# Optimization experiments

Measured on AMD Instinct MI355X. Metric: run time of the kernel, lower is better.

## Reference

```python
import jax, jax.numpy as jnp
import numpy as np

B, C, H, W = 8, 128, 64, 64
INTER = C // 2

def setup_inputs() -> dict:
    key = jax.random.key(0)
    ks = jax.random.split(key, 9)
    s = 0.05
    return {
        "x": jax.random.normal(ks[0], (B, C, H, W), dtype=jnp.float32),
        "theta_w": jax.random.normal(ks[1], (INTER, C), dtype=jnp.float32) * s,
        "theta_b": jax.random.normal(ks[2], (INTER,), dtype=jnp.float32) * s,
        "phi_w": jax.random.normal(ks[3], (INTER, C), dtype=jnp.float32) * s,
        "phi_b": jax.random.normal(ks[4], (INTER,), dtype=jnp.float32) * s,
        "g_w": jax.random.normal(ks[5], (INTER, C), dtype=jnp.float32) * s,
        "g_b": jax.random.normal(ks[6], (INTER,), dtype=jnp.float32) * s,
        "out_w": jax.random.normal(ks[7], (C, INTER), dtype=jnp.float32) * s,
        "out_b": jax.random.normal(ks[8], (C,), dtype=jnp.float32) * s,
    }

def reference(x, theta_w, theta_b, phi_w, phi_b, g_w, g_b, out_w, out_b):
    b, c, h, w = x.shape
    xf = x.reshape(b, c, h * w)                                   # [b, C, n]
    # 1x1 convs == per-pixel channel matmuls
    theta = jnp.einsum('oc,bcn->bno', theta_w, xf) + theta_b       # [b, n, inter]
    phi = jnp.einsum('oc,bcn->bon', phi_w, xf) + phi_b[:, None]    # [b, inter, n]
    g = jnp.einsum('oc,bcn->bno', g_w, xf) + g_b                   # [b, n, inter]
    attn = jax.nn.softmax(jnp.einsum('bno,bom->bnm', theta, phi), axis=-1)  # [b, n, n]
    y = jnp.einsum('bnm,bmo->bon', attn, g)                        # [b, inter, n]
    out = jnp.einsum('oc,bcn->bon', out_w, y) + out_b[:, None]     # [b, C, n]
    return out.reshape(b, c, h, w) + x
```

## Files before the change

kernel.cpp:

```cpp
#include <hip/hip_runtime.h>
#include <hip/hip_bf16.h>
#include <cstdint>
#include <cmath>

#define N_PIX 4096
#define CH    128
#define DD    64
#define NBATCH 8
#define NT    32

typedef unsigned short u16;
typedef __attribute__((ext_vector_type(8))) short bf8_t;
typedef __attribute__((ext_vector_type(4))) float f4_t;
typedef __attribute__((ext_vector_type(16))) float f16v;
typedef uint32_t u32x4 __attribute__((ext_vector_type(4)));
typedef uint32_t u32x2 __attribute__((ext_vector_type(2)));

#define L2E 1.44269504088896340736f

#if __has_builtin(__builtin_amdgcn_exp2f)
  #define EXP2(x) __builtin_amdgcn_exp2f(x)
#else
  #define EXP2(x) exp2f(x)
#endif

__device__ __forceinline__ u16 f2b(float f) {
  return __builtin_bit_cast(u16, __float2bfloat16(f));
}
__device__ __forceinline__ float b2f(u16 h) {
  union { uint32_t u; float f; } v; v.u = ((uint32_t)h) << 16;
  return v.f;
}
__device__ __forceinline__ uint32_t pack2(float a, float b) {
  return (uint32_t)f2b(a) | ((uint32_t)f2b(b) << 16);
}
__device__ __forceinline__ float max3f(float a, float b, float c) {
  return fmaxf(fmaxf(a, b), c);
}
__device__ __forceinline__ f4_t mfma16(bf8_t a, bf8_t b, f4_t c) {
  return __builtin_amdgcn_mfma_f32_16x16x32_bf16(a, b, c, 0, 0, 0);
}
__device__ __forceinline__ f16v mfma32(bf8_t a, bf8_t b, f16v c) {
  return __builtin_amdgcn_mfma_f32_32x32x16_bf16(a, b, c, 0, 0, 0);
}
__device__ __forceinline__ void pl32swap(uint32_t &a, uint32_t &b) {
  u32x2 r = __builtin_amdgcn_permlane32_swap(a, b, false, false);
  a = r[0];
  b = r[1];
}

__global__ __launch_bounds__(256) void proj_kernel(
    const float* __restrict__ x,
    const float* __restrict__ tw, const float* __restrict__ tb,
    const float* __restrict__ pw, const float* __restrict__ pb,
    const float* __restrict__ gw, const float* __restrict__ gb,
    u16* __restrict__ theta_h, u16* __restrict__ phi_h, u16* __restrict__ gt_h) {
  __shared__ __align__(16) u16 xT[64][136];
  const int blk = blockIdx.x;
  const int b  = blk >> 6;
  const int n0 = (blk & 63) << 6;
  const int tid = threadIdx.x;

  #pragma unroll
  for (int i = 0; i < 8; ++i) {
    int idx = tid + i * 256;
    int px = (idx & 15) * 4;
    int c  = idx >> 4;
    float4 v = *(const float4*)(x + ((size_t)b * CH + c) * N_PIX + n0 + px);
    xT[px + 0][c] = f2b(v.x);
    xT[px + 1][c] = f2b(v.y);
    xT[px + 2][c] = f2b(v.z);
    xT[px + 3][c] = f2b(v.w);
  }
  __syncthreads();

  const int lane = tid & 63;
  const int w    = tid >> 6;
  const int l4   = lane >> 4, l15 = lane & 15;

  bf8_t bw[3][4];
  float bias[3];
  #pragma unroll
  for (int nt = 0; nt < 3; ++nt) {
    int op = 16 * (3 * w + nt) + l15;
    const float* wrow; float bv; float scl;
    if (op < 64)       { wrow = tw + op * CH;          bv = tb[op];        scl = L2E; }
    else if (op < 128) { wrow = pw + (op - 64) * CH;   bv = pb[op - 64];   scl = 1.f; }
    else               { wrow = gw + (op - 128) * CH;  bv = gb[op - 128];  scl = 1.f; }
    bias[nt] = bv * scl;
    #pragma unroll
    for (int ks = 0; ks < 4; ++ks) {
      const float* p = wrow + 32 * ks + l4 * 8;
      bf8_t v;
      #pragma unroll
      for (int j = 0; j < 8; ++j) v[j] = (short)f2b(p[j] * scl);
      bw[nt][ks] = v;
    }
  }

  f4_t acc[4][3];
  #pragma unroll
  for (int mt = 0; mt < 4; ++mt)
    #pragma unroll
    for (int nt = 0; nt < 3; ++nt) acc[mt][nt] = (f4_t){0.f, 0.f, 0.f, 0.f};

  #pragma unroll
  for (int mt = 0; mt < 4; ++mt) {
    #pragma unroll
    for (int ks = 0; ks < 4; ++ks) {
      bf8_t a = *(const bf8_t*)&xT[l15 + 16 * mt][32 * ks + l4 * 8];
      #pragma unroll
      for (int nt = 0; nt < 3; ++nt)
        acc[mt][nt] = mfma16(a, bw[nt][ks], acc[mt][nt]);
    }
  }

  #pragma unroll
  for (int nt = 0; nt < 3; ++nt) {
    int op = 16 * (3 * w + nt) + l15;
    #pragma unroll
    for (int mt = 0; mt < 4; ++mt) {
      #pragma unroll
      for (int r = 0; r < 4; ++r) {
        int q = n0 + 16 * mt + l4 * 4 + r;
        u16 h = f2b(acc[mt][nt][r] + bias[nt]);
        if (op < 64)       theta_h[((size_t)b * N_PIX + q) * DD + op] = h;
        else if (op < 128) phi_h[((size_t)b * N_PIX + q) * DD + (op - 64)] = h;
        else               gt_h[((size_t)b * DD + (op - 128)) * N_PIX + q] = h;
      }
    }
  }
}

__global__ __launch_bounds__(512, 4) void attn_kernel(
    const u16* __restrict__ theta_h, const u16* __restrict__ phi_h,
    const u16* __restrict__ gt_h, u16* __restrict__ y_h) {
  __shared__ __align__(16) u16 smem[32768];

  const int bid = blockIdx.x;
  const int lb  = (bid & 7) * 64 + (bid >> 3);
  const int b   = lb >> 6;
  const int q0  = (lb & 63) << 6;
  const int tid = threadIdx.x;
  const int l   = tid & 63;
  const int w   = tid >> 6;
  const int qg  = w & 1;
  const int mh  = w >> 1;
  const int l31 = l & 31;
  const int hi  = l >> 5;

  bf8_t th[4];
  {
    const u16* trow = theta_h + ((size_t)b * N_PIX + q0 + 32 * qg + l31) * DD;
    #pragma unroll
    for (int kk = 0; kk < 4; ++kk)
      th[kk] = *(const bf8_t*)(trow + 16 * kk + 8 * hi);
  }

  const bf8_t onesA = __builtin_bit_cast(bf8_t,
      (u32x4){0x3F803F80u, 0x3F803F80u, 0x3F803F80u, 0x3F803F80u});

  f16v yacc[2];
  #pragma unroll
  for (int ot = 0; ot < 2; ++ot)
    #pragma unroll
    for (int r = 0; r < 16; ++r) yacc[ot][r] = 0.f;
  f16v y2;
  #pragma unroll
  for (int r = 0; r < 16; ++r) y2[r] = 0.f;
  float m_ = -1e30f;

  const int pr  = tid >> 3, pc = tid & 7;
  const int go  = tid >> 4, gc = tid & 15;
  const u16* phA = phi_h + ((size_t)b * N_PIX + pr) * DD + pc * 8;
  const u16* gtA = gt_h + ((size_t)b * DD + go) * N_PIX + gc * 8;
  const int pO0 = pr * 64 + ((pc ^ (pr & 7)) << 3);
  const int pO1 = pO0 + 4096;
  const int gO0 = 8192 + go * 128 + ((gc ^ (go & 7)) << 3);
  const int gO1 = gO0 + 4096;

  uint4 v0, v1, v2, v3;
  #define LOADS(kb_) do {                                              \
    v0 = *(const uint4*)(phA + (size_t)(kb_) * 8192);                  \
    v1 = *(const uint4*)(phA + (size_t)(kb_) * 8192 + 4096);           \
    v2 = *(const uint4*)(gtA + (size_t)(kb_) * 128);                   \
    v3 = *(const uint4*)(gtA + (size_t)(kb_) * 128 + 32 * (size_t)N_PIX); \
  } while (0)
  #define WRITES(buf_) do {                                            \
    u16* base_ = smem + (buf_) * 16384;                                \
    *(uint4*)(base_ + pO0) = v0;                                       \
    *(uint4*)(base_ + pO1) = v1;                                       \
    *(uint4*)(base_ + gO0) = v2;                                       \
    *(uint4*)(base_ + gO1) = v3;                                       \
  } while (0)

  LOADS(0); WRITES(0);
  __syncthreads();

  const int prow  = 32 * mh + l31;
  const int pbase = prow * 64;
  const int pkey  = prow & 7;

  #pragma unroll 2
  for (int t = 0; t < NT; ++t) {
    const int cur = t & 1;
    if (t < NT - 1) LOADS(t + 1);
    const u16* pb = smem + cur * 16384;
    const u16* gb = pb + 8192;

    f16v st;
    #pragma unroll
    for (int r = 0; r < 16; ++r) st[r] = 0.f;
    __builtin_amdgcn_s_setprio(1);
    #pragma unroll
    for (int kk = 0; kk < 4; ++kk) {
      bf8_t a = *(const bf8_t*)(pb + pbase + (((2 * kk + hi) ^ pkey) << 3));
      st = mfma32(a, th[kk], st);
    }
    __builtin_amdgcn_s_setprio(0);

    float t0 = max3f(st[0],  st[1],  st[2]);
    float t1 = max3f(st[3],  st[4],  st[5]);
    float t2 = max3f(st[6],  st[7],  st[8]);
    float t3 = max3f(st[9],  st[10], st[11]);
    float t4 = max3f(st[12], st[13], st[14]);
    float pmax = fmaxf(max3f(t0, t1, t2), max3f(t3, t4, st[15]));
    pmax = fmaxf(pmax, __shfl_xor(pmax, 32));

    if (!__all(pmax <= m_ + 8.f)) {
      float mn = fmaxf(m_, pmax);
      float sc = EXP2(m_ - mn);
      m_ = mn;
      y2[0] *= sc;
      #pragma unroll
      for (int ot = 0; ot < 2; ++ot)
        #pragma unroll
        for (int r = 0; r < 16; ++r) yacc[ot][r] *= sc;
    }

    #pragma unroll
    for (int r = 0; r < 16; ++r) st[r] = EXP2(st[r] - m_);

    uint32_t c0 = pack2(st[0],  st[1]),  c1 = pack2(st[2],  st[3]);
    uint32_t c2 = pack2(st[4],  st[5]),  c3 = pack2(st[6],  st[7]);
    uint32_t c4 = pack2(st[8],  st[9]),  c5 = pack2(st[10], st[11]);
    uint32_t c6 = pack2(st[12], st[13]), c7 = pack2(st[14], st[15]);
    pl32swap(c0, c2); pl32swap(c1, c3);
    pl32swap(c4, c6); pl32swap(c5, c7);
    bf8_t pf0 = __builtin_bit_cast(bf8_t, (u32x4){c0, c1, c2, c3});
    bf8_t pf1 = __builtin_bit_cast(bf8_t, (u32x4){c4, c5, c6, c7});

    __builtin_amdgcn_s_setprio(1);
    y2 = mfma32(onesA, pf0, y2);
    y2 = mfma32(onesA, pf1, y2);
    #pragma unroll
    for (int ot = 0; ot < 2; ++ot) {
      int orow  = 32 * ot + l31;
      int obase = orow * 128;
      int okey  = orow & 7;
      bf8_t g0 = *(const bf8_t*)(gb + obase + ((((mh << 2) + hi)     ^ okey) << 3));
      yacc[ot] = mfma32(g0, pf0, yacc[ot]);
      bf8_t g1 = *(const bf8_t*)(gb + obase + ((((mh << 2) + 2 + hi) ^ okey) << 3));
      yacc[ot] = mfma32(g1, pf1, yacc[ot]);
    }
    __builtin_amdgcn_s_setprio(0);

    if (t < NT - 1) WRITES(cur ^ 1);
    __syncthreads();
  }
  #undef LOADS
  #undef WRITES

  float l_ = y2[0];

  #pragma unroll
  for (int ot = 0; ot < 2; ++ot)
    #pragma unroll
    for (int r = 0; r < 16; ++r) {
      int o = 32 * ot + (r & 3) + 8 * (r >> 2) + 4 * hi;
      smem[(((qg * 4 + mh) * 64 + o) << 5) + l31] = f2b(yacc[ot][r]);
    }
  float* ml = (float*)(smem + 16384);
  if (hi == 0) {
    ml[(qg * 4 + mh) * 64 + l31]      = m_;
    ml[(qg * 4 + mh) * 64 + 32 + l31] = l_;
  }
  __syncthreads();

  {
    const int qg2 = tid >> 8;
    const int rem = tid & 255;
    const int qq  = rem & 31;
    const int og  = rem >> 5;
    float mi[4], li[4];
    #pragma unroll
    for (int i = 0; i < 4; ++i) {
      mi[i] = ml[(qg2 * 4 + i) * 64 + qq];
      li[i] = ml[(qg2 * 4 + i) * 64 + 32 + qq];
    }
    float M = fmaxf(fmaxf(mi[0], mi[1]), fmaxf(mi[2], mi[3]));
    float e[4], L = 0.f;
    #pragma unroll
    for (int i = 0; i < 4; ++i) { e[i] = EXP2(mi[i] - M); L += li[i] * e[i]; }
    float invL = 1.0f / L;
    float acc[8];
    #pragma unroll
    for (int oo = 0; oo < 8; ++oo) {
      int o = og * 8 + oo;
      float a = 0.f;
      #pragma unroll
      for (int i = 0; i < 4; ++i)
        a += b2f(smem[(((qg2 * 4 + i) * 64 + o) << 5) + qq]) * e[i];
      acc[oo] = a * invL;
    }
    uint4 ov;
    ov.x = pack2(acc[0], acc[1]);
    ov.y = pack2(acc[2], acc[3]);
    ov.z = pack2(acc[4], acc[5]);
    ov.w = pack2(acc[6], acc[7]);
    *(uint4*)(y_h + ((size_t)b * N_PIX + q0 + 32 * qg2 + qq) * DD + og * 8) = ov;
  }
}

__global__ __launch_bounds__(256) void outproj_kernel(
    const u16* __restrict__ y_h, const float* __restrict__ ow,
    const float* __restrict__ ob, const float* __restrict__ x,
    float* __restrict__ out) {
  __shared__ __align__(16) float ot[128][68];
  const int blk = blockIdx.x;
  const int b  = blk >> 6;
  const int n0 = (blk & 63) << 6;
  const int tid = threadIdx.x;
  const int lane = tid & 63;
  const int w    = tid >> 6;
  const int l4   = lane >> 4, l15 = lane & 15;

  bf8_t bw[2][2];
  float bias[2];
  #pragma unroll
  for (int nt = 0; nt < 2; ++nt) {
    int c = 16 * (2 * w + nt) + l15;
    bias[nt] = ob[c];
    #pragma unroll
    for (int ks = 0; ks < 2; ++ks) {
      const float* p = ow + c * DD + 32 * ks + l4 * 8;
      bf8_t v;
      #pragma unroll
      for (int j = 0; j < 8; ++j) v[j] = (short)f2b(p[j]);
      bw[nt][ks] = v;
    }
  }

  f4_t acc[4][2];
  #pragma unroll
  for (int mt = 0; mt < 4; ++mt)
    #pragma unroll
    for (int nt = 0; nt < 2; ++nt) acc[mt][nt] = (f4_t){0.f, 0.f, 0.f, 0.f};

  #pragma unroll
  for (int mt = 0; mt < 4; ++mt) {
    const u16* yr = y_h + ((size_t)b * N_PIX + n0 + 16 * mt + l15) * DD + l4 * 8;
    bf8_t a0 = *(const bf8_t*)yr;
    bf8_t a1 = *(const bf8_t*)(yr + 32);
    #pragma unroll
    for (int nt = 0; nt < 2; ++nt) {
      acc[mt][nt] = mfma16(a0, bw[nt][0], acc[mt][nt]);
      acc[mt][nt] = mfma16(a1, bw[nt][1], acc[mt][nt]);
    }
  }

  #pragma unroll
  for (int nt = 0; nt < 2; ++nt) {
    int c = 16 * (2 * w + nt) + l15;
    #pragma unroll
    for (int mt = 0; mt < 4; ++mt)
      #pragma unroll
      for (int r = 0; r < 4; ++r)
        ot[c][16 * mt + l4 * 4 + r] = acc[mt][nt][r] + bias[nt];
  }
  __syncthreads();

  #pragma unroll
  for (int i = 0; i < 8; ++i) {
    int idx = tid + i * 256;
    int px = (idx & 15) * 4;
    int c  = idx >> 4;
    size_t gi = ((size_t)b * CH + c) * N_PIX + n0 + px;
    float4 xv = *(const float4*)(x + gi);
    float4 o;
    o.x = ot[c][px + 0] + xv.x;
    o.y = ot[c][px + 1] + xv.y;
    o.z = ot[c][px + 2] + xv.z;
    o.w = ot[c][px + 3] + xv.w;
    *(float4*)(out + gi) = o;
  }
}

extern "C" void kernel_launch(void* const* d_in, const int* in_sizes, int n_in,
                              void* d_out, int out_size, void* d_ws, size_t ws_size,
                              hipStream_t stream) {
  const float* x  = (const float*)d_in[0];
  const float* tw = (const float*)d_in[1];
  const float* tb = (const float*)d_in[2];
  const float* pw = (const float*)d_in[3];
  const float* pb = (const float*)d_in[4];
  const float* gw = (const float*)d_in[5];
  const float* gb = (const float*)d_in[6];
  const float* ow = (const float*)d_in[7];
  const float* ob = (const float*)d_in[8];
  float* out = (float*)d_out;

  const size_t sz = (size_t)NBATCH * N_PIX * DD;
  u16* theta_h = (u16*)d_ws;
  u16* phi_h   = theta_h + sz;
  u16* gt_h    = phi_h + sz;
  u16* y_h     = gt_h + sz;

  proj_kernel<<<512, 256, 0, stream>>>(x, tw, tb, pw, pb, gw, gb, theta_h, phi_h, gt_h);
  attn_kernel<<<512, 512, 0, stream>>>(theta_h, phi_h, gt_h, y_h);
  outproj_kernel<<<512, 256, 0, stream>>>(y_h, ow, ob, x, out);
}
```

Measured before the change: 83.69 us.

## Deepen global-load prefetch to two tiles ahead with dual register sets

Replaces the single-register-set prefetch (load tile t+1 while computing t) with two register sets so global loads are issued two tiles ahead. Each loop iteration now processes two tiles, alternating between the two shared-memory buffers. This gives global loads more time to land before their values are written to shared memory, at the cost of extra VGPRs, which may lower occupancy.

```diff
diff --git a/kernel.cpp b/kernel.cpp
--- a/kernel.cpp
+++ b/kernel.cpp
@@ -179,33 +179,41 @@
   const int gO0 = 8192 + go * 128 + ((gc ^ (go & 7)) << 3);
   const int gO1 = gO0 + 4096;
 
-  uint4 v0, v1, v2, v3;
-  #define LOADS(kb_) do {                                              \
-    v0 = *(const uint4*)(phA + (size_t)(kb_) * 8192);                  \
-    v1 = *(const uint4*)(phA + (size_t)(kb_) * 8192 + 4096);           \
-    v2 = *(const uint4*)(gtA + (size_t)(kb_) * 128);                   \
-    v3 = *(const uint4*)(gtA + (size_t)(kb_) * 128 + 32 * (size_t)N_PIX); \
+  uint4 a0, a1, a2, a3;
+  uint4 b0, b1, b2, b3;
+  #define LOADS_A(kb_) do {                                            \
+    a0 = *(const uint4*)(phA + (size_t)(kb_) * 8192);                  \
+    a1 = *(const uint4*)(phA + (size_t)(kb_) * 8192 + 4096);           \
+    a2 = *(const uint4*)(gtA + (size_t)(kb_) * 128);                   \
+    a3 = *(const uint4*)(gtA + (size_t)(kb_) * 128 + 32 * (size_t)N_PIX); \
   } while (0)
-  #define WRITES(buf_) do {                                            \
+  #define LOADS_B(kb_) do {                                            \
+    b0 = *(const uint4*)(phA + (size_t)(kb_) * 8192);                  \
+    b1 = *(const uint4*)(phA + (size_t)(kb_) * 8192 + 4096);           \
+    b2 = *(const uint4*)(gtA + (size_t)(kb_) * 128);                   \
+    b3 = *(const uint4*)(gtA + (size_t)(kb_) * 128 + 32 * (size_t)N_PIX); \
+  } while (0)
+  #define WRITES_A(buf_) do {                                          \
     u16* base_ = smem + (buf_) * 16384;                                \
-    *(uint4*)(base_ + pO0) = v0;                                       \
-    *(uint4*)(base_ + pO1) = v1;                                       \
-    *(uint4*)(base_ + gO0) = v2;                                       \
-    *(uint4*)(base_ + gO1) = v3;                                       \
+    *(uint4*)(base_ + pO0) = a0;                                       \
+    *(uint4*)(base_ + pO1) = a1;                                       \
+    *(uint4*)(base_ + gO0) = a2;                                       \
+    *(uint4*)(base_ + gO1) = a3;                                       \
   } while (0)
-
-  LOADS(0); WRITES(0);
-  __syncthreads();
+  #define WRITES_B(buf_) do {                                          \
+    u16* base_ = smem + (buf_) * 16384;                                \
+    *(uint4*)(base_ + pO0) = b0;                                       \
+    *(uint4*)(base_ + pO1) = b1;                                       \
+    *(uint4*)(base_ + gO0) = b2;                                       \
+    *(uint4*)(base_ + gO1) = b3;                                       \
+  } while (0)
 
   const int prow  = 32 * mh + l31;
   const int pbase = prow * 64;
   const int pkey  = prow & 7;
 
-  #pragma unroll 2
-  for (int t = 0; t < NT; ++t) {
-    const int cur = t & 1;
-    if (t < NT - 1) LOADS(t + 1);
-    const u16* pb = smem + cur * 16384;
+  auto phase = [&](const int bufoff) {
+    const u16* pb = smem + bufoff;
     const u16* gb = pb + 8192;
 
     f16v st;
@@ -264,12 +272,27 @@
       yacc[ot] = mfma32(g1, pf1, yacc[ot]);
     }
     __builtin_amdgcn_s_setprio(0);
-
-    if (t < NT - 1) WRITES(cur ^ 1);
+  };
+
+  LOADS_A(0); WRITES_A(0);
+  LOADS_A(1);
+  LOADS_B(2);
+  __syncthreads();
+
+  for (int tt = 0; tt < NT; tt += 2) {
+    phase(0);
+    WRITES_A(1);
+    if (tt + 3 < NT) LOADS_A(tt + 3);
     __syncthreads();
-  }
-  #undef LOADS
-  #undef WRITES
+    phase(16384);
+    if (tt + 2 < NT) WRITES_B(0);
+    if (tt + 4 < NT) LOADS_B(tt + 4);
+    __syncthreads();
+  }
+  #undef LOADS_A
+  #undef LOADS_B
+  #undef WRITES_A
+  #undef WRITES_B
 
   float l_ = y2[0];
 
```

Result: slower. 97.21 us (+16.2%).

## Fuse output projection and residual into attention kernel epilogue

Applied to the files above, without the earlier changes.

Removes the separate outproj kernel by keeping the normalized attention output y in shared memory and doing the 64->128 output projection with 32x32 MFMAs inside the attention kernel, then adding bias and the residual x directly. This drops one kernel launch and the global write and read of y. In exchange, every attention block reloads and converts the out_w weights from global memory. The final stores go one float per lane along pixel rows, which is less vectorized than the old float4 path.

```diff
diff --git a/kernel.cpp b/kernel.cpp
--- a/kernel.cpp
+++ b/kernel.cpp
@@ -134,7 +134,9 @@
 
 __global__ __launch_bounds__(512, 4) void attn_kernel(
     const u16* __restrict__ theta_h, const u16* __restrict__ phi_h,
-    const u16* __restrict__ gt_h, u16* __restrict__ y_h) {
+    const u16* __restrict__ gt_h,
+    const float* __restrict__ ow, const float* __restrict__ ob,
+    const float* __restrict__ x, float* __restrict__ out) {
   __shared__ __align__(16) u16 smem[32768];
 
   const int bid = blockIdx.x;
@@ -287,6 +289,7 @@
   }
   __syncthreads();
 
+  u16* y_lds = smem + 17408;
   {
     const int qg2 = tid >> 8;
     const int rem = tid & 255;
@@ -318,81 +321,31 @@
     ov.y = pack2(acc[2], acc[3]);
     ov.z = pack2(acc[4], acc[5]);
     ov.w = pack2(acc[6], acc[7]);
-    *(uint4*)(y_h + ((size_t)b * N_PIX + q0 + 32 * qg2 + qq) * DD + og * 8) = ov;
-  }
-}
-
-__global__ __launch_bounds__(256) void outproj_kernel(
-    const u16* __restrict__ y_h, const float* __restrict__ ow,
-    const float* __restrict__ ob, const float* __restrict__ x,
-    float* __restrict__ out) {
-  __shared__ __align__(16) float ot[128][68];
-  const int blk = blockIdx.x;
-  const int b  = blk >> 6;
-  const int n0 = (blk & 63) << 6;
-  const int tid = threadIdx.x;
-  const int lane = tid & 63;
-  const int w    = tid >> 6;
-  const int l4   = lane >> 4, l15 = lane & 15;
-
-  bf8_t bw[2][2];
-  float bias[2];
-  #pragma unroll
-  for (int nt = 0; nt < 2; ++nt) {
-    int c = 16 * (2 * w + nt) + l15;
-    bias[nt] = ob[c];
-    #pragma unroll
-    for (int ks = 0; ks < 2; ++ks) {
-      const float* p = ow + c * DD + 32 * ks + l4 * 8;
-      bf8_t v;
-      #pragma unroll
-      for (int j = 0; j < 8; ++j) v[j] = (short)f2b(p[j]);
-      bw[nt][ks] = v;
-    }
-  }
-
-  f4_t acc[4][2];
-  #pragma unroll
-  for (int mt = 0; mt < 4; ++mt)
-    #pragma unroll
-    for (int nt = 0; nt < 2; ++nt) acc[mt][nt] = (f4_t){0.f, 0.f, 0.f, 0.f};
-
-  #pragma unroll
-  for (int mt = 0; mt < 4; ++mt) {
-    const u16* yr = y_h + ((size_t)b * N_PIX + n0 + 16 * mt + l15) * DD + l4 * 8;
-    bf8_t a0 = *(const bf8_t*)yr;
-    bf8_t a1 = *(const bf8_t*)(yr + 32);
-    #pragma unroll
-    for (int nt = 0; nt < 2; ++nt) {
-      acc[mt][nt] = mfma16(a0, bw[nt][0], acc[mt][nt]);
-      acc[mt][nt] = mfma16(a1, bw[nt][1], acc[mt][nt]);
-    }
-  }
-
-  #pragma unroll
-  for (int nt = 0; nt < 2; ++nt) {
-    int c = 16 * (2 * w + nt) + l15;
-    #pragma unroll
-    for (int mt = 0; mt < 4; ++mt)
-      #pragma unroll
-      for (int r = 0; r < 4; ++r)
-        ot[c][16 * mt + l4 * 4 + r] = acc[mt][nt][r] + bias[nt];
+    *(uint4*)(y_lds + (32 * qg2 + qq) * 72 + og * 8) = ov;
   }
   __syncthreads();
 
-  #pragma unroll
-  for (int i = 0; i < 8; ++i) {
-    int idx = tid + i * 256;
-    int px = (idx & 15) * 4;
-    int c  = idx >> 4;
-    size_t gi = ((size_t)b * CH + c) * N_PIX + n0 + px;
-    float4 xv = *(const float4*)(x + gi);
-    float4 o;
-    o.x = ot[c][px + 0] + xv.x;
-    o.y = ot[c][px + 1] + xv.y;
-    o.z = ot[c][px + 2] + xv.z;
-    o.w = ot[c][px + 3] + xv.w;
-    *(float4*)(out + gi) = o;
+  {
+    const int ct = w & 3;
+    const int qt = w >> 2;
+    f16v oacc;
+    #pragma unroll
+    for (int r = 0; r < 16; ++r) oacc[r] = 0.f;
+    #pragma unroll
+    for (int kk = 0; kk < 4; ++kk) {
+      const float* wp = ow + (size_t)(32 * ct + l31) * DD + 16 * kk + 8 * hi;
+      bf8_t av;
+      #pragma unroll
+      for (int j = 0; j < 8; ++j) av[j] = (short)f2b(wp[j]);
+      bf8_t bv = *(const bf8_t*)(y_lds + (32 * qt + l31) * 72 + 16 * kk + 8 * hi);
+      oacc = mfma32(av, bv, oacc);
+    }
+    #pragma unroll
+    for (int r = 0; r < 16; ++r) {
+      int c = 32 * ct + (r & 3) + 8 * (r >> 2) + 4 * hi;
+      size_t gi = ((size_t)b * CH + c) * N_PIX + q0 + 32 * qt + l31;
+      out[gi] = oacc[r] + ob[c] + x[gi];
+    }
   }
 }
 
@@ -414,9 +367,8 @@
   u16* theta_h = (u16*)d_ws;
   u16* phi_h   = theta_h + sz;
   u16* gt_h    = phi_h + sz;
-  u16* y_h     = gt_h + sz;
-
-  proj_kernel<<<512, 256, 0, stream>>>(x, tw, tb, pw, pb, gw, gb, theta_h, phi_h, gt_h);
-  attn_kernel<<<512, 512, 0, stream>>>(theta_h, phi_h, gt_h, y_h);
-  outproj_kernel<<<512, 256, 0, stream>>>(y_h, ow, ob, x, out);
-}
+
+  proj_kernel<<<512, 256, 0, stream>>>(x, tw, tb, pw, pb, gw, gb,
+                                       theta_h, phi_h, gt_h);
+  attn_kernel<<<512, 512, 0, stream>>>(theta_h, phi_h, gt_h, ow, ob, x, out);
+}
```

New measurement: 79.94 us. 1.05x faster.
